# Optimization experiments

Measured on AMD Instinct MI355X. Metric: run time of the kernel, lower is better.

## Reference

```python
import jax, jax.numpy as jnp
import numpy as np

N_NODES = 100000
N_EDGES = 1600000
LN_EPS = 1e-5
CLAMP = 1.8


def setup_inputs() -> dict:
    key = jax.random.key(0)
    ks = jax.random.split(key, 12)
    feats = [100, 64, 64, 47]
    inp = {
        "x": jax.random.normal(ks[0], (N_NODES, feats[0]), dtype=jnp.float32),
        "adj_vals": jax.random.uniform(ks[1], (N_EDGES,), dtype=jnp.float32),
        "adj_row": jax.random.randint(ks[2], (N_EDGES,), 0, N_NODES),
        "adj_col": jax.random.randint(ks[3], (N_EDGES,), 0, N_NODES),
        "ln_gamma": jnp.ones((feats[0],), dtype=jnp.float32),
        "ln_beta": jnp.zeros((feats[0],), dtype=jnp.float32),
    }
    for i in range(3):
        fi, fo = feats[i], feats[i + 1]
        bound = 1.0 / np.sqrt(fi)
        inp[f"W{i+1}"] = jax.random.uniform(ks[4 + 2 * i], (fi, fo), minval=-bound, maxval=bound, dtype=jnp.float32)
        inp[f"b{i+1}"] = jax.random.uniform(ks[5 + 2 * i], (fo,), minval=-bound, maxval=bound, dtype=jnp.float32)
    return inp


def _spmm(vals, row, col, x):
    # out[i] = sum_{e: row[e]==i} vals[e] * x[col[e]]
    gathered = vals[:, None] * x[col]  # [E, D]
    return jax.ops.segment_sum(gathered, row, num_segments=N_NODES)


def reference(x, adj_vals, adj_row, adj_col, ln_gamma, ln_beta, W1, b1, W2, b2, W3, b3):
    # clamp to [-1.8, 1.8]: relu(x+1.8)-1.8 then 1.8-relu(1.8-x)
    x = jnp.clip(x, -CLAMP, CLAMP)
    # LayerNorm over last dim (100)
    mu = jnp.mean(x, axis=-1, keepdims=True)
    var = jnp.mean(jnp.square(x - mu), axis=-1, keepdims=True)
    x = (x - mu) * jax.lax.rsqrt(var + LN_EPS) * ln_gamma + ln_beta
    # GCN layers: Linear -> spmm -> (elu except last); dropout=0 => identity
    x = jax.nn.elu(_spmm(adj_vals, adj_row, adj_col, x @ W1 + b1))
    x = jax.nn.elu(_spmm(adj_vals, adj_row, adj_col, x @ W2 + b2))
    x = _spmm(adj_vals, adj_row, adj_col, x @ W3 + b3)
    return x
```

## Files before the change

### kernel.cpp

```cpp
#include <hip/hip_runtime.h>
#include <cstdint>
#include <cstddef>

#define N_NODES_C 100000
#define N_EDGES_C 1600000
#define LN_EPS_C 1e-5f
#define CLAMP_C 1.8f
#define LN_BLOCKS 1024
#define BINS 98
#define CHUNK 4096
#define EPT 16
#define NCHUNK 391

typedef unsigned short ushort_t;

__device__ __forceinline__ float readlane_f(float v, int l) {
  return __uint_as_float(__builtin_amdgcn_readlane(__float_as_uint(v), l));
}

__device__ __forceinline__ float wave_sum(float v) {
#pragma unroll
  for (int off = 32; off > 0; off >>= 1) v += __shfl_xor(v, off, 64);
  return v;
}

__device__ __forceinline__ ushort_t f2bf(float f) {
  unsigned u = __float_as_uint(f);
  unsigned r = (u + 0x7fffu + ((u >> 16) & 1u)) >> 16;
  return (ushort_t)r;
}
__device__ __forceinline__ float bf2f(ushort_t u) {
  return __uint_as_float((unsigned)u << 16);
}

__global__ __launch_bounds__(256) void hist_kernel(const int* __restrict__ row,
                                                   int* __restrict__ counts) {
  int tid = blockIdx.x * blockDim.x + threadIdx.x;
  int nt = gridDim.x * blockDim.x;
  int r[8];
#pragma unroll
  for (int k = 0; k < 8; ++k) {
    int e = tid + k * nt;
    r[k] = (e < N_EDGES_C) ? row[e] : -1;
  }
#pragma unroll
  for (int k = 0; k < 8; ++k)
    if (r[k] >= 0) atomicAdd(&counts[r[k]], 1);
}

__global__ void scan1_kernel(const int* __restrict__ counts, int* __restrict__ rowstart,
                             int* __restrict__ bsums) {
  __shared__ int lds[256];
  int t = threadIdx.x;
  int base = blockIdx.x * 1024 + t * 4;
  int c0 = (base + 0 < N_NODES_C) ? counts[base + 0] : 0;
  int c1 = (base + 1 < N_NODES_C) ? counts[base + 1] : 0;
  int c2 = (base + 2 < N_NODES_C) ? counts[base + 2] : 0;
  int c3 = (base + 3 < N_NODES_C) ? counts[base + 3] : 0;
  int s = c0 + c1 + c2 + c3;
  lds[t] = s;
  __syncthreads();
#pragma unroll
  for (int off = 1; off < 256; off <<= 1) {
    int v = (t >= off) ? lds[t - off] : 0;
    __syncthreads();
    lds[t] += v;
    __syncthreads();
  }
  int incl = lds[t];
  int excl = incl - s;
  if (t == 255) bsums[blockIdx.x] = incl;
  if (base + 0 < N_NODES_C) rowstart[base + 0] = excl;
  excl += c0;
  if (base + 1 < N_NODES_C) rowstart[base + 1] = excl;
  excl += c1;
  if (base + 2 < N_NODES_C) rowstart[base + 2] = excl;
  excl += c2;
  if (base + 3 < N_NODES_C) rowstart[base + 3] = excl;
}

__global__ void scan2_kernel(int* __restrict__ bsums, int nb) {
  __shared__ int lds[128];
  int t = threadIdx.x;
  int v = (t < nb) ? bsums[t] : 0;
  lds[t] = v;
  __syncthreads();
#pragma unroll
  for (int off = 1; off < 128; off <<= 1) {
    int u = (t >= off) ? lds[t - off] : 0;
    __syncthreads();
    lds[t] += u;
    __syncthreads();
  }
  if (t < nb) bsums[t] = lds[t] - v;
}

__global__ void scan3_kernel(int* __restrict__ rowstart, int* __restrict__ cursor,
                             int* __restrict__ bincur, const int* __restrict__ bsums) {
  int add = bsums[blockIdx.x];
  int base = blockIdx.x * 1024 + threadIdx.x * 4;
#pragma unroll
  for (int i = 0; i < 4; ++i) {
    int rI = base + i;
    if (rI < N_NODES_C) {
      int v = rowstart[rI] + add;
      rowstart[rI] = v;
      cursor[rI] = v;
      if ((rI & 1023) == 0) bincur[rI >> 10] = v;
    }
  }
}

__global__ __launch_bounds__(256) void partition_kernel(
    const int* __restrict__ row, const int* __restrict__ col,
    const float* __restrict__ vals, int* __restrict__ bincur,
    int2* __restrict__ stage_cv, int* __restrict__ stage_r) {
  __shared__ int hist[128];
  __shared__ int scanarr[128];
  __shared__ int cnt2[128];
  __shared__ int basearr[128];
  __shared__ int2 s_cv[CHUNK];
  __shared__ int s_r[CHUNK];
  __shared__ unsigned char s_bin[CHUNK];
  int t = threadIdx.x;
  int e0 = blockIdx.x * CHUNK;
  if (t < 128) {
    hist[t] = 0;
    cnt2[t] = 0;
    basearr[t] = 0;
  }
  __syncthreads();
  int rr[EPT], cc[EPT], bn[EPT];
  float vv[EPT];
#pragma unroll
  for (int k = 0; k < EPT; ++k) {
    int e = e0 + t + k * 256;
    bool valid = e < N_EDGES_C;
    rr[k] = valid ? row[e] : -1;
    cc[k] = valid ? col[e] : 0;
    vv[k] = valid ? vals[e] : 0.f;
  }
#pragma unroll
  for (int k = 0; k < EPT; ++k) {
    bn[k] = (rr[k] >= 0) ? (rr[k] >> 10) : -1;
    if (bn[k] >= 0) atomicAdd(&hist[bn[k]], 1);
  }
  __syncthreads();
  if (t < 128) scanarr[t] = hist[t];
  __syncthreads();
#pragma unroll
  for (int off = 1; off < 128; off <<= 1) {
    int u = 0;
    if (t < 128 && t >= off) u = scanarr[t - off];
    __syncthreads();
    if (t < 128) scanarr[t] += u;
    __syncthreads();
  }
  if (t < BINS && hist[t] > 0) basearr[t] = atomicAdd(&bincur[t], hist[t]);
#pragma unroll
  for (int k = 0; k < EPT; ++k) {
    if (bn[k] >= 0) {
      int lstart = scanarr[bn[k]] - hist[bn[k]];
      int slot = lstart + atomicAdd(&cnt2[bn[k]], 1);
      s_cv[slot] = make_int2(cc[k], __float_as_int(vv[k]));
      s_r[slot] = rr[k];
      s_bin[slot] = (unsigned char)bn[k];
    }
  }
  __syncthreads();
  int totv = scanarr[127];
  for (int s = t; s < totv; s += 256) {
    int b = s_bin[s];
    int lstart = scanarr[b] - hist[b];
    int g = basearr[b] + (s - lstart);
    stage_cv[g] = s_cv[s];
    stage_r[g] = s_r[s];
  }
}

__global__ __launch_bounds__(256) void binscatter_ln_kernel(
    const int2* __restrict__ stage_cv, const int* __restrict__ stage_r,
    int* __restrict__ cursor, int2* __restrict__ edges_s,
    const float* __restrict__ x, const float* __restrict__ gamma,
    const float* __restrict__ beta, const float* __restrict__ W1,
    const float* __restrict__ b1, ushort_t* __restrict__ y) {
  if ((blockIdx.x & 1) == 0) {
    int i0 = (blockIdx.x >> 1) * 2048;
    if (i0 >= N_EDGES_C) return;
    int t = threadIdx.x;
    int2 cv[8];
    int rn[8], p[8];
    bool in[8];
#pragma unroll
    for (int k = 0; k < 8; ++k) {
      int i = i0 + t + k * 256;
      in[k] = i < N_EDGES_C;
      cv[k] = in[k] ? stage_cv[i] : make_int2(0, 0);
      rn[k] = in[k] ? stage_r[i] : 0;
    }
#pragma unroll
    for (int k = 0; k < 8; ++k)
      if (in[k]) p[k] = atomicAdd(&cursor[rn[k]], 1);
#pragma unroll
    for (int k = 0; k < 8; ++k)
      if (in[k]) edges_s[p[k]] = cv[k];
  } else {
    int lane = threadIdx.x & 63;
    int wid = (blockIdx.x >> 1) * 4 + (threadIdx.x >> 6);
    const int nw = LN_BLOCKS * 4;
    float bias = b1[lane];
    float g0 = gamma[lane];
    float be0 = beta[lane];
    float g1 = (lane < 36) ? gamma[64 + lane] : 0.f;
    float be1 = (lane < 36) ? beta[64 + lane] : 0.f;
    for (int n = wid; n < N_NODES_C; n += nw) {
      const float* xr = x + (size_t)n * 100;
      float x0 = xr[lane];
      float x1 = (lane < 36) ? xr[64 + lane] : 0.f;
      x0 = fminf(fmaxf(x0, -CLAMP_C), CLAMP_C);
      x1 = fminf(fmaxf(x1, -CLAMP_C), CLAMP_C);
      float mu = wave_sum(x0 + x1) * 0.01f;
      float d0 = x0 - mu;
      float d1 = (lane < 36) ? (x1 - mu) : 0.f;
      float var = wave_sum(d0 * d0 + d1 * d1) * 0.01f;
      float inv = rsqrtf(var + LN_EPS_C);
      float xn0 = d0 * inv * g0 + be0;
      float xn1 = d1 * inv * g1 + be1;
      float acc = bias;
#pragma unroll
      for (int k = 0; k < 64; ++k) acc = fmaf(readlane_f(xn0, k), W1[k * 64 + lane], acc);
#pragma unroll
      for (int k = 0; k < 36; ++k) acc = fmaf(readlane_f(xn1, k), W1[(64 + k) * 64 + lane], acc);
      y[(size_t)n * 64 + lane] = f2bf(acc);
    }
  }
}

template <int DOUT>
__global__ __launch_bounds__(256) void spmm_elu_gemm_kernel(
    const int* __restrict__ rowstart, const int* __restrict__ counts,
    const int2* __restrict__ edges_s, const ushort_t* __restrict__ yb,
    const float* __restrict__ W, const float* __restrict__ b,
    ushort_t* __restrict__ out) {
  int lane = threadIdx.x & 63;
  int wid = blockIdx.x * (blockDim.x >> 6) + (threadIdx.x >> 6);
  int nw = gridDim.x * (blockDim.x >> 6);
  float w[64];
#pragma unroll
  for (int k = 0; k < 64; ++k) w[k] = (lane < DOUT) ? W[k * DOUT + lane] : 0.f;
  float bias = (lane < DOUT) ? b[lane] : 0.f;
  for (int n = wid; n < N_NODES_C; n += nw) {
    int start = rowstart[n];
    int cnt = counts[n];
    float a[8];
#pragma unroll
    for (int u = 0; u < 8; ++u) a[u] = 0.f;
    for (int base = 0; base < cnt; base += 64) {
      int m = cnt - base;
      if (m > 64) m = 64;
      int2 ev = make_int2(0, 0);
      if (lane < m) ev = edges_s[start + base + lane];
      int mr = (m + 15) & ~15;
      for (int j = 0; j < mr; j += 16) {
        float g[16];
#pragma unroll
        for (int u = 0; u < 16; ++u)
          g[u] = bf2f(yb[(size_t)__builtin_amdgcn_readlane(ev.x, j + u) * 64 + lane]);
#pragma unroll
        for (int u = 0; u < 16; ++u)
          a[u & 7] = fmaf(
              __uint_as_float(__builtin_amdgcn_readlane((unsigned)ev.y, j + u)), g[u],
              a[u & 7]);
      }
    }
    float acc = ((a[0] + a[1]) + (a[2] + a[3])) + ((a[4] + a[5]) + (a[6] + a[7]));
    float xe = (acc > 0.f) ? acc : expm1f(acc);
    float o = bias;
#pragma unroll
    for (int k = 0; k < 64; ++k) o = fmaf(readlane_f(xe, k), w[k], o);
    if (lane < DOUT) out[(size_t)n * 64 + lane] = f2bf(o);
  }
}

__global__ __launch_bounds__(256) void spmm_final_kernel(
    const int* __restrict__ rowstart, const int* __restrict__ counts,
    const int2* __restrict__ edges_s, const ushort_t* __restrict__ yb,
    float* __restrict__ out) {
  int lane = threadIdx.x & 63;
  int wid = blockIdx.x * (blockDim.x >> 6) + (threadIdx.x >> 6);
  int nw = gridDim.x * (blockDim.x >> 6);
  int lmask = (lane < 47) ? lane : 46;
  for (int n = wid; n < N_NODES_C; n += nw) {
    int start = rowstart[n];
    int cnt = counts[n];
    float a[8];
#pragma unroll
    for (int u = 0; u < 8; ++u) a[u] = 0.f;
    for (int base = 0; base < cnt; base += 64) {
      int m = cnt - base;
      if (m > 64) m = 64;
      int2 ev = make_int2(0, 0);
      if (lane < m) ev = edges_s[start + base + lane];
      int mr = (m + 15) & ~15;
      for (int j = 0; j < mr; j += 16) {
        float g[16];
#pragma unroll
        for (int u = 0; u < 16; ++u)
          g[u] = bf2f(yb[(size_t)__builtin_amdgcn_readlane(ev.x, j + u) * 64 + lmask]);
#pragma unroll
        for (int u = 0; u < 16; ++u)
          a[u & 7] = fmaf(
              __uint_as_float(__builtin_amdgcn_readlane((unsigned)ev.y, j + u)), g[u],
              a[u & 7]);
      }
    }
    float acc = ((a[0] + a[1]) + (a[2] + a[3])) + ((a[4] + a[5]) + (a[6] + a[7]));
    if (lane < 47) out[(size_t)n * 47 + lane] = acc;
  }
}

extern "C" void kernel_launch(void* const* d_in, const int* in_sizes, int n_in,
                              void* d_out, int out_size, void* d_ws, size_t ws_size,
                              hipStream_t stream) {
  const float* x = (const float*)d_in[0];
  const float* adj_vals = (const float*)d_in[1];
  const int* adj_row = (const int*)d_in[2];
  const int* adj_col = (const int*)d_in[3];
  const float* gamma = (const float*)d_in[4];
  const float* beta = (const float*)d_in[5];
  const float* W1 = (const float*)d_in[6];
  const float* b1 = (const float*)d_in[7];
  const float* W2 = (const float*)d_in[8];
  const float* b2 = (const float*)d_in[9];
  const float* W3 = (const float*)d_in[10];
  const float* b3 = (const float*)d_in[11];
  float* out = (float*)d_out;

  char* ws = (char*)d_ws;
  size_t off = 0;
  auto alloc = [&](size_t bytes) -> void* {
    void* p = ws + off;
    off += (bytes + 255) & ~(size_t)255;
    return p;
  };
  ushort_t* bufA = (ushort_t*)alloc(sizeof(ushort_t) * (size_t)N_NODES_C * 64);
  ushort_t* bufB = (ushort_t*)alloc(sizeof(ushort_t) * (size_t)N_NODES_C * 64);
  int* counts = (int*)alloc(sizeof(int) * N_NODES_C);
  int* cursor = (int*)alloc(sizeof(int) * N_NODES_C);
  int* rowstart = (int*)alloc(sizeof(int) * N_NODES_C);
  int* bsums = (int*)alloc(sizeof(int) * 256);
  int* bincur = (int*)alloc(sizeof(int) * 128);
  int2* edges_s = (int2*)alloc(sizeof(int2) * N_EDGES_C);
  int2* stage_cv = (int2*)alloc(sizeof(int2) * N_EDGES_C);
  int* stage_r = (int*)alloc(sizeof(int) * N_EDGES_C);

  hipMemsetAsync(counts, 0, sizeof(int) * N_NODES_C, stream);

  hist_kernel<<<782, 256, 0, stream>>>(adj_row, counts);
  int nb = (N_NODES_C + 1023) / 1024;
  scan1_kernel<<<nb, 256, 0, stream>>>(counts, rowstart, bsums);
  scan2_kernel<<<1, 128, 0, stream>>>(bsums, nb);
  scan3_kernel<<<nb, 256, 0, stream>>>(rowstart, cursor, bincur, bsums);

  partition_kernel<<<NCHUNK, 256, 0, stream>>>(adj_row, adj_col, adj_vals, bincur,
                                               stage_cv, stage_r);
  binscatter_ln_kernel<<<2048, 256, 0, stream>>>(
      stage_cv, stage_r, cursor, edges_s, x, gamma, beta, W1, b1, bufA);

  spmm_elu_gemm_kernel<64><<<2048, 256, 0, stream>>>(rowstart, counts, edges_s, bufA,
                                                     W2, b2, bufB);
  spmm_elu_gemm_kernel<47><<<2048, 256, 0, stream>>>(rowstart, counts, edges_s, bufB,
                                                     W3, b3, bufA);
  spmm_final_kernel<<<2048, 256, 0, stream>>>(rowstart, counts, edges_s, bufA, out);
}
```

Measured before the change: 422.7 us.

## Use finer 256-row bins and per-bin blocks for localized scatter

Partitioning now groups edges into 391 bins of 256 rows instead of 98 bins of 1024 rows, so each bin's cursor and destination range is smaller. The bin-scatter stage assigns one block per bin and walks that bin's contiguous edge range, which keeps cursor atomics and edges_s writes within a narrow address window for better cache locality. The partition kernel scans 512 bins in LDS and recomputes the bin from the row instead of storing it. The cost is a longer scan in the partition kernel and possible load imbalance if some bins hold many more edges.

```diff
diff --git a/kernel.cpp b/kernel.cpp
--- a/kernel.cpp
+++ b/kernel.cpp
@@ -7,7 +7,8 @@
 #define LN_EPS_C 1e-5f
 #define CLAMP_C 1.8f
 #define LN_BLOCKS 1024
-#define BINS 98
+#define BINS 391
+#define BIN_SHIFT 8
 #define CHUNK 4096
 #define EPT 16
 #define NCHUNK 391
@@ -106,7 +107,7 @@
       int v = rowstart[rI] + add;
       rowstart[rI] = v;
       cursor[rI] = v;
-      if ((rI & 1023) == 0) bincur[rI >> 10] = v;
+      if ((rI & 255) == 0) bincur[rI >> BIN_SHIFT] = v;
     }
   }
 }
@@ -115,19 +116,18 @@
     const int* __restrict__ row, const int* __restrict__ col,
     const float* __restrict__ vals, int* __restrict__ bincur,
     int2* __restrict__ stage_cv, int* __restrict__ stage_r) {
-  __shared__ int hist[128];
-  __shared__ int scanarr[128];
-  __shared__ int cnt2[128];
-  __shared__ int basearr[128];
+  __shared__ int hist[512];
+  __shared__ int scanarr[512];
+  __shared__ int cnt2[512];
+  __shared__ int basearr[512];
   __shared__ int2 s_cv[CHUNK];
   __shared__ int s_r[CHUNK];
-  __shared__ unsigned char s_bin[CHUNK];
   int t = threadIdx.x;
   int e0 = blockIdx.x * CHUNK;
-  if (t < 128) {
-    hist[t] = 0;
-    cnt2[t] = 0;
-    basearr[t] = 0;
+  for (int b = t; b < 512; b += 256) {
+    hist[b] = 0;
+    cnt2[b] = 0;
+    basearr[b] = 0;
   }
   __syncthreads();
   int rr[EPT], cc[EPT], bn[EPT];
@@ -142,21 +142,34 @@
   }
 #pragma unroll
   for (int k = 0; k < EPT; ++k) {
-    bn[k] = (rr[k] >= 0) ? (rr[k] >> 10) : -1;
+    bn[k] = (rr[k] >= 0) ? (rr[k] >> BIN_SHIFT) : -1;
     if (bn[k] >= 0) atomicAdd(&hist[bn[k]], 1);
   }
   __syncthreads();
-  if (t < 128) scanarr[t] = hist[t];
-  __syncthreads();
-#pragma unroll
-  for (int off = 1; off < 128; off <<= 1) {
-    int u = 0;
-    if (t < 128 && t >= off) u = scanarr[t - off];
-    __syncthreads();
-    if (t < 128) scanarr[t] += u;
-    __syncthreads();
-  }
-  if (t < BINS && hist[t] > 0) basearr[t] = atomicAdd(&bincur[t], hist[t]);
+  scanarr[t] = hist[t];
+  __syncthreads();
+#pragma unroll
+  for (int off = 1; off < 256; off <<= 1) {
+    int u = (t >= off) ? scanarr[t - off] : 0;
+    __syncthreads();
+    scanarr[t] += u;
+    __syncthreads();
+  }
+  scanarr[256 + t] = hist[256 + t];
+  __syncthreads();
+#pragma unroll
+  for (int off = 1; off < 256; off <<= 1) {
+    int u = (t >= off) ? scanarr[256 + t - off] : 0;
+    __syncthreads();
+    scanarr[256 + t] += u;
+    __syncthreads();
+  }
+  int tot0 = scanarr[255];
+  __syncthreads();
+  scanarr[256 + t] += tot0;
+  __syncthreads();
+  for (int b = t; b < BINS; b += 256)
+    if (hist[b] > 0) basearr[b] = atomicAdd(&bincur[b], hist[b]);
 #pragma unroll
   for (int k = 0; k < EPT; ++k) {
     if (bn[k] >= 0) {
@@ -164,13 +177,12 @@
       int slot = lstart + atomicAdd(&cnt2[bn[k]], 1);
       s_cv[slot] = make_int2(cc[k], __float_as_int(vv[k]));
       s_r[slot] = rr[k];
-      s_bin[slot] = (unsigned char)bn[k];
-    }
-  }
-  __syncthreads();
-  int totv = scanarr[127];
+    }
+  }
+  __syncthreads();
+  int totv = scanarr[511];
   for (int s = t; s < totv; s += 256) {
-    int b = s_bin[s];
+    int b = s_r[s] >> BIN_SHIFT;
     int lstart = scanarr[b] - hist[b];
     int g = basearr[b] + (s - lstart);
     stage_cv[g] = s_cv[s];
@@ -179,34 +191,38 @@
 }
 
 __global__ __launch_bounds__(256) void binscatter_ln_kernel(
-    const int2* __restrict__ stage_cv, const int* __restrict__ stage_r,
-    int* __restrict__ cursor, int2* __restrict__ edges_s,
+    const int* __restrict__ rowstart, const int2* __restrict__ stage_cv,
+    const int* __restrict__ stage_r, int* __restrict__ cursor,
+    int2* __restrict__ edges_s,
     const float* __restrict__ x, const float* __restrict__ gamma,
     const float* __restrict__ beta, const float* __restrict__ W1,
     const float* __restrict__ b1, ushort_t* __restrict__ y) {
-  if ((blockIdx.x & 1) == 0) {
-    int i0 = (blockIdx.x >> 1) * 2048;
-    if (i0 >= N_EDGES_C) return;
+  if (blockIdx.x < BINS) {
+    int b = blockIdx.x;
     int t = threadIdx.x;
-    int2 cv[8];
-    int rn[8], p[8];
-    bool in[8];
-#pragma unroll
-    for (int k = 0; k < 8; ++k) {
-      int i = i0 + t + k * 256;
-      in[k] = i < N_EDGES_C;
-      cv[k] = in[k] ? stage_cv[i] : make_int2(0, 0);
-      rn[k] = in[k] ? stage_r[i] : 0;
-    }
-#pragma unroll
-    for (int k = 0; k < 8; ++k)
-      if (in[k]) p[k] = atomicAdd(&cursor[rn[k]], 1);
-#pragma unroll
-    for (int k = 0; k < 8; ++k)
-      if (in[k]) edges_s[p[k]] = cv[k];
+    int lo = rowstart[b << BIN_SHIFT];
+    int hi = (b == BINS - 1) ? N_EDGES_C : rowstart[(b + 1) << BIN_SHIFT];
+    for (int i0 = lo; i0 < hi; i0 += 2048) {
+      int2 cv[8];
+      int rn[8], p[8];
+      bool in[8];
+#pragma unroll
+      for (int k = 0; k < 8; ++k) {
+        int i = i0 + t + k * 256;
+        in[k] = i < hi;
+        cv[k] = in[k] ? stage_cv[i] : make_int2(0, 0);
+        rn[k] = in[k] ? stage_r[i] : 0;
+      }
+#pragma unroll
+      for (int k = 0; k < 8; ++k)
+        if (in[k]) p[k] = atomicAdd(&cursor[rn[k]], 1);
+#pragma unroll
+      for (int k = 0; k < 8; ++k)
+        if (in[k]) edges_s[p[k]] = cv[k];
+    }
   } else {
     int lane = threadIdx.x & 63;
-    int wid = (blockIdx.x >> 1) * 4 + (threadIdx.x >> 6);
+    int wid = ((int)blockIdx.x - BINS) * 4 + (threadIdx.x >> 6);
     const int nw = LN_BLOCKS * 4;
     float bias = b1[lane];
     float g0 = gamma[lane];
@@ -349,7 +365,7 @@
   int* cursor = (int*)alloc(sizeof(int) * N_NODES_C);
   int* rowstart = (int*)alloc(sizeof(int) * N_NODES_C);
   int* bsums = (int*)alloc(sizeof(int) * 256);
-  int* bincur = (int*)alloc(sizeof(int) * 128);
+  int* bincur = (int*)alloc(sizeof(int) * 512);
   int2* edges_s = (int2*)alloc(sizeof(int2) * N_EDGES_C);
   int2* stage_cv = (int2*)alloc(sizeof(int2) * N_EDGES_C);
   int* stage_r = (int*)alloc(sizeof(int) * N_EDGES_C);
@@ -364,8 +380,8 @@
 
   partition_kernel<<<NCHUNK, 256, 0, stream>>>(adj_row, adj_col, adj_vals, bincur,
                                                stage_cv, stage_r);
-  binscatter_ln_kernel<<<2048, 256, 0, stream>>>(
-      stage_cv, stage_r, cursor, edges_s, x, gamma, beta, W1, b1, bufA);
+  binscatter_ln_kernel<<<BINS + LN_BLOCKS, 256, 0, stream>>>(
+      rowstart, stage_cv, stage_r, cursor, edges_s, x, gamma, beta, W1, b1, bufA);
 
   spmm_elu_gemm_kernel<64><<<2048, 256, 0, stream>>>(rowstart, counts, edges_s, bufA,
                                                      W2, b2, bufB);
```

New measurement: 412.1 us. -2.5%, faster.
